# Kernel tuning notes

Hardware: AMD Instinct MI355X
Metric: run time of the kernel (lower is better)

## Reference

```python
import jax, jax.numpy as jnp
import numpy as np

B, T = 16, 512
LAT, ACT, TSK = 512, 64, 96
E, NH, HD = 1024, 16, 64
L, HID, MAXS = 4, 4096, 512


def setup_inputs() -> dict:
    key = jax.random.key(0)
    ks = jax.random.split(key, 16)
    def rn(k, shape, std=0.02):
        return jax.random.normal(k, shape, jnp.float32) * std
    return {
        "z": jax.random.normal(ks[0], (B, T, LAT), jnp.float32),
        "a": jax.random.normal(ks[1], (B, T, ACT), jnp.float32),
        "task_emb": jax.random.normal(ks[2], (B, T, TSK), jnp.float32),
        "input_proj_w": rn(ks[3], (LAT + ACT + TSK, E)),
        "input_proj_b": jnp.zeros((E,), jnp.float32),
        "pos_emb": rn(ks[4], (1, MAXS, E)),
        "ln1_w": jnp.ones((L, E), jnp.float32),
        "ln1_b": jnp.zeros((L, E), jnp.float32),
        "qkv_w": rn(ks[5], (L, E, 3 * E)),
        "proj_w": rn(ks[6], (L, E, E)),
        "proj_b": jnp.zeros((L, E), jnp.float32),
        "ln2_w": jnp.ones((L, E), jnp.float32),
        "ln2_b": jnp.zeros((L, E), jnp.float32),
        "mlp_w1": rn(ks[7], (L, E, HID)),
        "mlp_b1": jnp.zeros((L, HID), jnp.float32),
        "mlp_w2": rn(ks[8], (L, HID, E)),
        "mlp_b2": jnp.zeros((L, E), jnp.float32),
        "out_norm_w": jnp.ones((E,), jnp.float32),
        "out_norm_b": jnp.zeros((E,), jnp.float32),
        "delta_w": rn(ks[9], (E, LAT)),
        "delta_b": jnp.zeros((LAT,), jnp.float32),
    }


def _ln(x, w, b, eps=1e-5):
    mu = jnp.mean(x, -1, keepdims=True)
    var = jnp.mean((x - mu) ** 2, -1, keepdims=True)
    return (x - mu) * jax.lax.rsqrt(var + eps) * w + b


def reference(z, a, task_emb, input_proj_w, input_proj_b, pos_emb,
              ln1_w, ln1_b, qkv_w, proj_w, proj_b, ln2_w, ln2_b,
              mlp_w1, mlp_b1, mlp_w2, mlp_b2,
              out_norm_w, out_norm_b, delta_w, delta_b):
    Bv, Tv, _ = z.shape
    x = jnp.concatenate([z, a, task_emb], axis=-1) @ input_proj_w + input_proj_b
    x = x + pos_emb[:, :Tv]
    scale = HD ** -0.5
    causal = jnp.tril(jnp.ones((Tv, Tv), bool))  # seq_start=0, no cache
    for l in range(L):
        h = _ln(x, ln1_w[l], ln1_b[l])
        qkv = (h @ qkv_w[l]).reshape(Bv, Tv, 3, NH, HD)
        q = jnp.swapaxes(qkv[:, :, 0], 1, 2) * scale  # (B,H,T,D)
        k = jnp.swapaxes(qkv[:, :, 1], 1, 2)
        v = jnp.swapaxes(qkv[:, :, 2], 1, 2)
        attn = jnp.einsum('bhqd,bhkd->bhqk', q, k)
        attn = jnp.where(causal, attn, -jnp.inf)
        attn = jax.nn.softmax(attn, axis=-1)
        o = jnp.einsum('bhqk,bhkd->bhqd', attn, v)
        o = jnp.swapaxes(o, 1, 2).reshape(Bv, Tv, E)
        x = x + (o @ proj_w[l] + proj_b[l])
        h2 = _ln(x, ln2_w[l], ln2_b[l])
        mid = jax.nn.gelu(h2 @ mlp_w1[l] + mlp_b1[l], approximate=False)
        x = x + (mid @ mlp_w2[l] + mlp_b2[l])
    x = _ln(x, out_norm_w, out_norm_b)
    return z + (x @ delta_w + delta_b)
```

## Files before the change

kernel.cpp:

```cpp
#include <hip/hip_runtime.h>
#include <hip/hip_bf16.h>
#include <math.h>

typedef unsigned short u16;
typedef unsigned int u32;
typedef __attribute__((ext_vector_type(4))) float f32x4;
typedef __attribute__((ext_vector_type(8))) short bf16x8;

#define DEV static __device__ __forceinline__

DEV u16 f2bf(float f) {
  __hip_bfloat16 h = __float2bfloat16(f);
  union { __hip_bfloat16 h; u16 u; } c; c.h = h; return c.u;
}

DEV float fast_gelu(float v) {
  float u = v * (1.5957691216f + 0.0713548162f * v * v);
  return v * __builtin_amdgcn_rcpf(1.f + __expf(-u));
}

DEV void gload16(const void* g, void* l) {
  __builtin_amdgcn_global_load_lds((const __attribute__((address_space(1))) u32*)g,
                                   (__attribute__((address_space(3))) u32*)l, 16, 0, 0);
}

__global__ void transpose_w(const float* __restrict__ src, u16* __restrict__ dst,
                            int R, int C, int Rp, size_t sstride, size_t dstride) {
  src += (size_t)blockIdx.z * sstride;
  dst += (size_t)blockIdx.z * dstride;
  __shared__ float tile[32][33];
  int tx = threadIdx.x, ty = threadIdx.y;
  int c0 = blockIdx.x * 32, r0 = blockIdx.y * 32;
  #pragma unroll
  for (int j = 0; j < 4; j++) {
    int r = r0 + ty + j * 8, c = c0 + tx;
    tile[ty + j * 8][tx] = (r < R && c < C) ? src[(size_t)r * C + c] : 0.f;
  }
  __syncthreads();
  #pragma unroll
  for (int j = 0; j < 4; j++) {
    int cc = c0 + ty + j * 8;
    int rr = r0 + tx;
    if (cc < C && rr < Rp) dst[(size_t)cc * Rp + rr] = f2bf(tile[tx][ty + j * 8]);
  }
}

__global__ void concat_k(const float* __restrict__ z, const float* __restrict__ a,
                         const float* __restrict__ te, u16* __restrict__ A) {
  const int total = 8192 * 704;
  for (int idx = blockIdx.x * 256 + threadIdx.x; idx < total; idx += gridDim.x * 256) {
    int m = idx / 704;
    int j = idx - m * 704;
    float v = 0.f;
    if (j < 512) v = z[(size_t)m * 512 + j];
    else if (j < 576) v = a[(size_t)m * 64 + (j - 512)];
    else if (j < 672) v = te[(size_t)m * 96 + (j - 576)];
    A[idx] = f2bf(v);
  }
}

__global__ __launch_bounds__(256) void ln_k(const float* __restrict__ x,
                                            const float* __restrict__ w,
                                            const float* __restrict__ b,
                                            u16* __restrict__ h) {
  int row = blockIdx.x * 4 + (threadIdx.x >> 6);
  int lane = threadIdx.x & 63;
  const float4* xr = (const float4*)(x + (size_t)row * 1024);
  float4 v[4]; float s = 0.f, sq = 0.f;
  #pragma unroll
  for (int i = 0; i < 4; i++) {
    v[i] = xr[lane + i * 64];
    s += v[i].x + v[i].y + v[i].z + v[i].w;
    sq += v[i].x * v[i].x + v[i].y * v[i].y + v[i].z * v[i].z + v[i].w * v[i].w;
  }
  #pragma unroll
  for (int off = 32; off >= 1; off >>= 1) { s += __shfl_xor(s, off); sq += __shfl_xor(sq, off); }
  float mean = s * (1.f / 1024.f);
  float var = sq * (1.f / 1024.f) - mean * mean;
  float rstd = rsqrtf(var + 1e-5f);
  const float4* wv = (const float4*)w;
  const float4* bv = (const float4*)b;
  u32* hr = (u32*)(h + (size_t)row * 1024);
  #pragma unroll
  for (int i = 0; i < 4; i++) {
    int idx = lane + i * 64;
    float4 wi = wv[idx], bi = bv[idx];
    float o0 = (v[i].x - mean) * rstd * wi.x + bi.x;
    float o1 = (v[i].y - mean) * rstd * wi.y + bi.y;
    float o2 = (v[i].z - mean) * rstd * wi.z + bi.z;
    float o3 = (v[i].w - mean) * rstd * wi.w + bi.w;
    hr[idx * 2]     = (u32)f2bf(o0) | ((u32)f2bf(o1) << 16);
    hr[idx * 2 + 1] = (u32)f2bf(o2) | ((u32)f2bf(o3) << 16);
  }
}

template <int FM, int EPI>
__global__ __launch_bounds__(512, 2) void gemm8(
    const u16* __restrict__ A, const u16* __restrict__ BT,
    float* __restrict__ outF, u16* __restrict__ outH,
    const float* __restrict__ bias, const float* __restrict__ res,
    const float* __restrict__ pos, int M, int N, int K, int gx) {
  constexpr int BM = FM * 32;
  constexpr int ABYTES = BM * 64;
  constexpr int BBYTES = 256 * 64;
  constexpr int SLICE = ABYTES + BBYTES;
  constexpr int LA = ABYTES / 8192;
  constexpr int LB = 2;
  __shared__ char lds[4 * SLICE];

  const int tid = threadIdx.x, lane = tid & 63, w = tid >> 6;
  const int wr = w >> 2, wc = w & 3;

  const int nwg = gridDim.x, orig = blockIdx.x;
  const int q = nwg >> 3, r = nwg & 7;
  const int xcd = orig & 7, loc = orig >> 3;
  const int sid = (xcd < r ? xcd * (q + 1) : r * (q + 1) + (xcd - r) * q) + loc;
  const int m0 = (sid / gx) * BM, n0 = (sid % gx) * 256;

  const char* Ag = (const char*)(A + (size_t)m0 * K);
  const char* Bg = (const char*)(BT + (size_t)n0 * K);
  const int Krow = K * 2;

  int aoff[LA], boff[LB];
  #pragma unroll
  for (int l = 0; l < LA; l++) {
    int c = l * 512 + tid, rw = c >> 2, g = (c & 3) ^ ((rw >> 1) & 3);
    aoff[l] = rw * Krow + g * 16;
  }
  #pragma unroll
  for (int l = 0; l < LB; l++) {
    int c = l * 512 + tid, rw = c >> 2, g = (c & 3) ^ ((rw >> 1) & 3);
    boff[l] = rw * Krow + g * 16;
  }
  const int ra = wr * (FM * 16) + (lane & 15);
  const int aRd = ra * 64 + (((lane >> 4) ^ ((ra >> 1) & 3)) << 4);
  const int rb = wc * 64 + (lane & 15);
  const int bRd = rb * 64 + (((lane >> 4) ^ ((rb >> 1) & 3)) << 4);

  f32x4 zero4 = {0.f, 0.f, 0.f, 0.f};
  f32x4 acc[FM][4];
  #pragma unroll
  for (int m = 0; m < FM; m++)
    #pragma unroll
    for (int n = 0; n < 4; n++) acc[m][n] = zero4;

  auto stageA = [&](int s) {
    char* Ad = lds + (s & 3) * SLICE;
    const char* src = Ag + (size_t)s * 64;
    #pragma unroll
    for (int l = 0; l < LA; l++)
      gload16(src + aoff[l], Ad + (l * 512 + w * 64) * 16);
  };
  auto stageB = [&](int s) {
    char* Bd = lds + (s & 3) * SLICE + ABYTES;
    const char* src = Bg + (size_t)s * 64;
    #pragma unroll
    for (int l = 0; l < LB; l++)
      gload16(src + boff[l], Bd + (l * 512 + w * 64) * 16);
  };

  const int NS = K >> 5;
  stageA(0); stageB(0); stageA(1); stageB(1);
  asm volatile("s_waitcnt vmcnt(3)" ::: "memory");
  __builtin_amdgcn_s_barrier();

  #pragma unroll 1
  for (int s = 0; s < NS; s++) {
    char* Ar = lds + (s & 3) * SLICE;
    char* Br = Ar + ABYTES;
    const bool pre = (s + 2 < NS);
    bf16x8 bfr[4], af[4];
    #pragma unroll
    for (int n = 0; n < 4; n++) bfr[n] = *(const bf16x8*)(Br + bRd + n * 1024);
    #pragma unroll
    for (int m = 0; m < 4; m++) af[m] = *(const bf16x8*)(Ar + aRd + m * 1024);
    if (pre) { stageA(s + 2); stageB(s + 2); }
    __builtin_amdgcn_sched_barrier(0);
    __builtin_amdgcn_s_barrier();
    asm volatile("s_waitcnt lgkmcnt(0)" ::: "memory");
    __builtin_amdgcn_sched_barrier(0);
    __builtin_amdgcn_s_setprio(1);
    #pragma unroll
    for (int m = 0; m < 4; m++)
      #pragma unroll
      for (int n = 0; n < 4; n++)
        acc[m][n] = __builtin_amdgcn_mfma_f32_16x16x32_bf16(af[m], bfr[n], acc[m][n], 0, 0, 0);
    __builtin_amdgcn_s_setprio(0);
    __builtin_amdgcn_sched_barrier(0);
    if (pre) asm volatile("s_waitcnt vmcnt(3)" ::: "memory");
    else     asm volatile("s_waitcnt vmcnt(0)" ::: "memory");
    __builtin_amdgcn_s_barrier();
  }

  #pragma unroll
  for (int m = 0; m < FM; m++) {
    #pragma unroll
    for (int i = 0; i < 4; i++) {
      int gm = m0 + wr * (FM * 16) + m * 16 + ((lane >> 4) << 2) + i;
      #pragma unroll
      for (int n = 0; n < 4; n++) {
        int gn = n0 + wc * 64 + n * 16 + (lane & 15);
        float v = acc[m][n][i];
        if (EPI & 1) v += bias[gn];
        if (EPI & 2) v += pos[(size_t)(gm & 511) * N + gn];
        if (EPI & 4) v += res[(size_t)gm * N + gn];
        if (EPI & 8) v = fast_gelu(v);
        if (EPI & 16) outH[(size_t)gm * N + gn] = f2bf(v);
        else outF[(size_t)gm * N + gn] = v;
      }
    }
  }
}

#define SB0 __builtin_amdgcn_sched_barrier(0)
#define VMW(N) asm volatile("s_waitcnt vmcnt(" #N ")" ::: "memory")
#define PH_TAIL(MFMAS) \
  SB0; __builtin_amdgcn_s_barrier(); \
  asm volatile("s_waitcnt lgkmcnt(0)" ::: "memory"); SB0; \
  __builtin_amdgcn_s_setprio(1); MFMAS; __builtin_amdgcn_s_setprio(0); \
  SB0; __builtin_amdgcn_s_barrier();
#define PH_TAILV(MFMAS, NN) \
  SB0; __builtin_amdgcn_s_barrier(); \
  asm volatile("s_waitcnt lgkmcnt(0)" ::: "memory"); SB0; \
  __builtin_amdgcn_s_setprio(1); MFMAS; __builtin_amdgcn_s_setprio(0); \
  SB0; VMW(NN); __builtin_amdgcn_s_barrier();
#define MM16(MB, BF) \
  _Pragma("unroll") \
  for (int mm = 0; mm < 4; mm++) \
    _Pragma("unroll") \
    for (int nn = 0; nn < 4; nn++) \
      acc[(MB) + mm][nn] = __builtin_amdgcn_mfma_f32_16x16x32_bf16(afr[mm][0], BF[nn], acc[(MB) + mm][nn], 0, 0, 0);
#define MM32(MB) \
  _Pragma("unroll") \
  for (int kk2 = 0; kk2 < 2; kk2++) \
    _Pragma("unroll") \
    for (int mm = 0; mm < 4; mm++) \
      _Pragma("unroll") \
      for (int nn = 0; nn < 4; nn++) \
        acc[(MB) + mm][nn] = __builtin_amdgcn_mfma_f32_16x16x32_bf16( \
            afr[mm][kk2], kk2 ? bfr1[nn] : bfr0[nn], acc[(MB) + mm][nn], 0, 0, 0);
#define RD_A1(BUF, K2L, MB) { \
  const char* _b = aRdB[BUF]; \
  afr[0][0] = *(const bf16x8*)(_b + aby[(MB) + 0][K2L]); \
  afr[1][0] = *(const bf16x8*)(_b + aby[(MB) + 1][K2L]); \
  afr[2][0] = *(const bf16x8*)(_b + aby[(MB) + 2][K2L]); \
  afr[3][0] = *(const bf16x8*)(_b + aby[(MB) + 3][K2L]); }
#define RD_A8(BUF, MB) { \
  const char* _b = aRdB[BUF]; \
  afr[0][0] = *(const bf16x8*)(_b + aby[(MB) + 0][0]); \
  afr[0][1] = *(const bf16x8*)(_b + aby[(MB) + 0][1]); \
  afr[1][0] = *(const bf16x8*)(_b + aby[(MB) + 1][0]); \
  afr[1][1] = *(const bf16x8*)(_b + aby[(MB) + 1][1]); \
  afr[2][0] = *(const bf16x8*)(_b + aby[(MB) + 2][0]); \
  afr[2][1] = *(const bf16x8*)(_b + aby[(MB) + 2][1]); \
  afr[3][0] = *(const bf16x8*)(_b + aby[(MB) + 3][0]); \
  afr[3][1] = *(const bf16x8*)(_b + aby[(MB) + 3][1]); }
#define RD_BALL(BUF) { \
  const char* _b = bRdB[BUF]; \
  bfr0[0] = *(const bf16x8*)(_b + bby[0][0]); bfr1[0] = *(const bf16x8*)(_b + bby[0][1]); \
  bfr0[1] = *(const bf16x8*)(_b + bby[1][0]); bfr1[1] = *(const bf16x8*)(_b + bby[1][1]); \
  bfr0[2] = *(const bf16x8*)(_b + bby[2][0]); bfr1[2] = *(const bf16x8*)(_b + bby[2][1]); \
  bfr0[3] = *(const bf16x8*)(_b + bby[3][0]); bfr1[3] = *(const bf16x8*)(_b + bby[3][1]); }

template <int FM, int EPI>
__global__ __launch_bounds__(512, 2) void gemmP(
    const u16* __restrict__ A, const u16* __restrict__ BT,
    float* __restrict__ outF, u16* __restrict__ outH,
    const float* __restrict__ bias, const float* __restrict__ res,
    const float* __restrict__ pos, int M, int N, int K, int gx) {
  constexpr int RB = 16384;
  constexpr int NAREG = (FM == 8 ? 4 : 2);
  constexpr int BOFF = NAREG * RB;
  __shared__ char lds[BOFF + 4 * RB];

  const int tid = threadIdx.x, lane = tid & 63, w = tid >> 6;
  const int wr = w >> 2, wc = w & 3;
  const int ln = lane & 15, g = lane >> 4;

  const int nwg = gridDim.x, orig = blockIdx.x;
  const int q = nwg >> 3, r = nwg & 7;
  const int xcd = orig & 7, loc = orig >> 3;
  const int sid = (xcd < r ? xcd * (q + 1) : r * (q + 1) + (xcd - r) * q) + loc;
  const int m0 = (sid / gx) * (FM * 32), n0 = (sid % gx) * 256;

  const char* Ag = (const char*)(A + (size_t)m0 * K);
  const char* Bg = (const char*)(BT + (size_t)n0 * K);
  const size_t K2 = (size_t)K * 2;
  const int NT = K >> 6, NTm1 = NT - 1, NI = NT >> 1;

  int aby[FM][2], bby[4][2];
  #pragma unroll
  for (int m = 0; m < FM; m++) {
    int rr = (FM == 8 ? 0 : wr * 64) + m * 16 + ln;
    #pragma unroll
    for (int k2 = 0; k2 < 2; k2++)
      aby[m][k2] = rr * 128 + (((k2 * 4 + g) ^ (rr & 7)) << 4);
  }
  #pragma unroll
  for (int n = 0; n < 4; n++) {
    int rr = (wc & 1) * 64 + n * 16 + ln;
    #pragma unroll
    for (int k2 = 0; k2 < 2; k2++)
      bby[n][k2] = rr * 128 + (((k2 * 4 + g) ^ (rr & 7)) << 4);
  }
  const char* aRdB[2];
  const char* bRdB[2];
  if constexpr (FM == 8) {
    aRdB[0] = lds + (0 * 2 + wr) * RB;
    aRdB[1] = lds + (1 * 2 + wr) * RB;
  } else {
    aRdB[0] = lds;
    aRdB[1] = lds + RB;
  }
  bRdB[0] = lds + BOFF + (0 * 2 + (wc >> 1)) * RB;
  bRdB[1] = lds + BOFF + (1 * 2 + (wc >> 1)) * RB;

  int soff[2], sdst[2];
  #pragma unroll
  for (int l = 0; l < 2; l++) {
    int c = l * 512 + tid, rw = c >> 3, sl = c & 7;
    soff[l] = rw * (int)K2 + ((sl ^ (rw & 7)) << 4);
    sdst[l] = (l * 512 + w * 64) * 16;
  }

  auto stA = [&](int buf, int tau, int h) {
    char* d = lds + (FM == 8 ? (buf * 2 + h) : buf) * RB;
    const char* s = Ag + (size_t)(tau < NT ? tau : NTm1) * 128 + (FM == 8 ? (size_t)h * 128 * K2 : 0);
    #pragma unroll
    for (int l = 0; l < 2; l++) gload16(s + soff[l], d + sdst[l]);
  };
  auto stB = [&](int buf, int tau, int gg) {
    char* d = lds + BOFF + (buf * 2 + gg) * RB;
    const char* s = Bg + (size_t)(tau < NT ? tau : NTm1) * 128 + (size_t)gg * 128 * K2;
    #pragma unroll
    for (int l = 0; l < 2; l++) gload16(s + soff[l], d + sdst[l]);
  };

  f32x4 zero4 = {0.f, 0.f, 0.f, 0.f};
  f32x4 acc[FM][4];
  #pragma unroll
  for (int m = 0; m < FM; m++)
    #pragma unroll
    for (int n = 0; n < 4; n++) acc[m][n] = zero4;

  bf16x8 afr[4][2], bfr0[4], bfr1[4];

  if constexpr (FM == 8) {
    stA(0, 0, 0); stA(0, 0, 1); stB(0, 0, 0); stB(0, 0, 1); stB(1, 1, 0); stB(1, 1, 1);
    VMW(4);
    __builtin_amdgcn_s_barrier();
    #pragma unroll 1
    for (int J = 0; J < NI; J++) {
      const int t = 2 * J;
      RD_BALL(0); RD_A8(0, 0); stA(1, t + 1, 0); stA(1, t + 1, 1);
      PH_TAIL(MM32(0));
      RD_A8(0, 4); stB(0, t + 2, 0); stB(0, t + 2, 1);
      PH_TAILV(MM32(4), 4);
      RD_BALL(1); RD_A8(1, 0); stA(0, t + 2, 0); stA(0, t + 2, 1);
      PH_TAIL(MM32(0));
      RD_A8(1, 4); stB(1, t + 3, 0); stB(1, t + 3, 1);
      PH_TAILV(MM32(4), 4);
    }
  } else {
    stA(0, 0, 0); stB(0, 0, 0); stB(0, 0, 1); stB(1, 1, 0); stB(1, 1, 1);
    VMW(4);
    __builtin_amdgcn_s_barrier();
    #pragma unroll 1
    for (int J = 0; J < NI; J++) {
      const int t = 2 * J;
      RD_BALL(0); RD_A1(0, 0, 0); stA(1, t + 1, 0);
      PH_TAIL(MM16(0, bfr0));
      RD_A1(0, 1, 0); stB(0, t + 2, 0);
      PH_TAILV(MM16(0, bfr1), 2);
      RD_BALL(1); RD_A1(1, 0, 0); stB(0, t + 2, 1); stA(0, t + 2, 0);
      PH_TAIL(MM16(0, bfr0));
      RD_A1(1, 1, 0); stB(1, t + 3, 0); stB(1, t + 3, 1);
      PH_TAILV(MM16(0, bfr1), 4);
    }
  }
  VMW(0);

  #pragma unroll
  for (int m = 0; m < FM; m++) {
    #pragma unroll
    for (int i = 0; i < 4; i++) {
      int gm = m0 + wr * (FM * 16) + m * 16 + (g << 2) + i;
      #pragma unroll
      for (int n = 0; n < 4; n++) {
        int gn = n0 + wc * 64 + n * 16 + ln;
        float v = acc[m][n][i];
        if (EPI & 1) v += bias[gn];
        if (EPI & 2) v += pos[(size_t)(gm & 511) * N + gn];
        if (EPI & 4) v += res[(size_t)gm * N + gn];
        if (EPI & 8) v = fast_gelu(v);
        if (EPI & 16) outH[(size_t)gm * N + gn] = f2bf(v);
        else outF[(size_t)gm * N + gn] = v;
      }
    }
  }
}
#undef RD_BALL
#undef RD_A8
#undef RD_A1
#undef MM32
#undef MM16
#undef PH_TAILV
#undef PH_TAIL
#undef VMW
#undef SB0

__global__ __launch_bounds__(512) void attn_k(const u16* __restrict__ qkv,
                                              u16* __restrict__ o) {
  __shared__ u16 Ks[512 * 64];
  __shared__ u16 Vt[64 * 512];
  __shared__ u16 Ps[8 * 1024];
  const int tid = threadIdx.x, lane = tid & 63, w = tid >> 6;
  const int b = blockIdx.x >> 4, h = blockIdx.x & 15;
  const u16* base = qkv + (size_t)b * 512 * 3072 + h * 64;
  const int ln = lane & 15, g = lane >> 4;

  #pragma unroll
  for (int it = 0; it < 8; it++) {
    int chunk = it * 512 + tid;
    int row = chunk >> 3;
    int ib = (chunk & 7) * 16;
    int lb = ib ^ ((row & 7) << 4);
    gload16((const char*)(base + 1024 + (size_t)row * 3072) + lb,
            (char*)Ks + (it * 512 + w * 64) * 16);
  }
  {
    const u16* vrow = base + 2048 + (size_t)tid * 3072;
    #pragma unroll
    for (int c = 0; c < 8; c++) {
      uint4 u = *(const uint4*)(vrow + c * 8);
      u32 vals[4] = {u.x, u.y, u.z, u.w};
      #pragma unroll
      for (int pc = 0; pc < 4; pc++) {
        int d0 = c * 8 + pc * 2;
        size_t by0 = ((size_t)d0 * 1024 + tid * 2) ^ (size_t)((d0 & 7) << 4);
        size_t by1 = ((size_t)(d0 + 1) * 1024 + tid * 2) ^ (size_t)(((d0 + 1) & 7) << 4);
        *(u16*)((char*)Vt + by0) = (u16)(vals[pc] & 0xffff);
        *(u16*)((char*)Vt + by1) = (u16)(vals[pc] >> 16);
      }
    }
  }
  __syncthreads();

  const int qts[4] = {w, 15 - w, 16 + w, 31 - w};
  #pragma unroll
  for (int qi = 0; qi < 4; qi++) {
    const int qt = qts[qi];
    const int q0 = qt * 16;
    const int qcol = q0 + ln;
    const u16* qrow = base + (size_t)(q0 + ln) * 3072 + (g << 3);
    bf16x8 qf0 = *(const bf16x8*)qrow;
    bf16x8 qf1 = *(const bf16x8*)(qrow + 32);
    f32x4 zero4 = {0.f, 0.f, 0.f, 0.f};
    f32x4 oA[4] = {zero4, zero4, zero4, zero4};
    float mrun = -INFINITY, lrun = 0.f;
    const int nch = (qt >> 2) + 1;
    for (int ch = 0; ch < nch; ch++) {
      const int kb = ch * 64;
      f32x4 st[4];
      #pragma unroll
      for (int s = 0; s < 4; s++) {
        st[s] = zero4;
        int krow = kb + s * 16 + ln;
        int byc = krow * 128 + (g << 4);
        int sw = (krow & 7) << 4;
        bf16x8 ka  = *(const bf16x8*)((const char*)Ks + (byc ^ sw));
        bf16x8 kb2 = *(const bf16x8*)((const char*)Ks + ((byc + 64) ^ sw));
        st[s] = __builtin_amdgcn_mfma_f32_16x16x32_bf16(ka, qf0, st[s], 0, 0, 0);
        st[s] = __builtin_amdgcn_mfma_f32_16x16x32_bf16(kb2, qf1, st[s], 0, 0, 0);
      }
      float sv[16]; float cmax = -INFINITY;
      #pragma unroll
      for (int s = 0; s < 4; s++) {
        #pragma unroll
        for (int i = 0; i < 4; i++) {
          int key0 = kb + s * 16 + (g << 2) + i;
          float v = st[s][i] * 0.125f;
          if (key0 > qcol) v = -INFINITY;
          sv[s * 4 + i] = v;
          cmax = fmaxf(cmax, v);
        }
      }
      cmax = fmaxf(cmax, __shfl_xor(cmax, 16));
      cmax = fmaxf(cmax, __shfl_xor(cmax, 32));
      float mnew = fmaxf(mrun, cmax);
      float corr = __expf(mrun - mnew);
      float pp[16]; float psum = 0.f;
      #pragma unroll
      for (int i = 0; i < 16; i++) { pp[i] = __expf(sv[i] - mnew); psum += pp[i]; }
      psum += __shfl_xor(psum, 16);
      psum += __shfl_xor(psum, 32);
      lrun = lrun * corr + psum;
      mrun = mnew;
      {
        int sw2 = (ln & 3) << 4;
        #pragma unroll
        for (int hh = 0; hh < 2; hh++) {
          int pbase = w * 2048 + hh * 1024 + ln * 64;
          uint2 t0, t1;
          t0.x = (u32)f2bf(pp[8 * hh + 0]) | ((u32)f2bf(pp[8 * hh + 1]) << 16);
          t0.y = (u32)f2bf(pp[8 * hh + 2]) | ((u32)f2bf(pp[8 * hh + 3]) << 16);
          t1.x = (u32)f2bf(pp[8 * hh + 4]) | ((u32)f2bf(pp[8 * hh + 5]) << 16);
          t1.y = (u32)f2bf(pp[8 * hh + 6]) | ((u32)f2bf(pp[8 * hh + 7]) << 16);
          *(uint2*)((char*)Ps + pbase + ((g << 3) ^ sw2)) = t0;
          *(uint2*)((char*)Ps + pbase + ((32 + (g << 3)) ^ sw2)) = t1;
        }
      }
      #pragma unroll
      for (int i = 0; i < 4; i++) {
        float fi = __shfl(corr, (g << 2) + i);
        oA[0][i] *= fi; oA[1][i] *= fi; oA[2][i] *= fi; oA[3][i] *= fi;
      }
      {
        int sw2 = (ln & 3) << 4;
        #pragma unroll
        for (int hh = 0; hh < 2; hh++) {
          bf16x8 pf = *(const bf16x8*)((const char*)Ps + w * 2048 + hh * 1024 +
                                       ln * 64 + ((g << 4) ^ sw2));
          #pragma unroll
          for (int n = 0; n < 4; n++) {
            int d = n * 16 + ln;
            int vby = (d * 1024 + (kb + 32 * hh + (g << 3)) * 2) ^ ((d & 7) << 4);
            bf16x8 vf = *(const bf16x8*)((const char*)Vt + vby);
            oA[n] = __builtin_amdgcn_mfma_f32_16x16x32_bf16(pf, vf, oA[n], 0, 0, 0);
          }
        }
      }
    }
    float inv = 1.f / lrun;
    #pragma unroll
    for (int i = 0; i < 4; i++) {
      float fi = __shfl(inv, (g << 2) + i);
      int qr = q0 + (g << 2) + i;
      size_t orow = ((size_t)b * 512 + qr) * 1024 + h * 64;
      #pragma unroll
      for (int n = 0; n < 4; n++)
        o[orow + n * 16 + ln] = f2bf(oA[n][i] * fi);
    }
  }
}

extern "C" void kernel_launch(void* const* d_in, const int* in_sizes, int n_in,
                              void* d_out, int out_size, void* d_ws, size_t ws_size,
                              hipStream_t stream) {
  const float* z    = (const float*)d_in[0];
  const float* a    = (const float*)d_in[1];
  const float* te   = (const float*)d_in[2];
  const float* ipw  = (const float*)d_in[3];
  const float* ipb  = (const float*)d_in[4];
  const float* pos  = (const float*)d_in[5];
  const float* ln1w = (const float*)d_in[6];
  const float* ln1b = (const float*)d_in[7];
  const float* qkvw = (const float*)d_in[8];
  const float* projw= (const float*)d_in[9];
  const float* projb= (const float*)d_in[10];
  const float* ln2w = (const float*)d_in[11];
  const float* ln2b = (const float*)d_in[12];
  const float* w1   = (const float*)d_in[13];
  const float* b1   = (const float*)d_in[14];
  const float* w2   = (const float*)d_in[15];
  const float* b2   = (const float*)d_in[16];
  const float* onw  = (const float*)d_in[17];
  const float* onb  = (const float*)d_in[18];
  const float* dw   = (const float*)d_in[19];
  const float* db   = (const float*)d_in[20];
  float* out = (float*)d_out;

  char* p = (char*)d_ws;
  auto alloc = [&](size_t bytes) -> char* {
    char* r = p; p += (bytes + 255) & ~(size_t)255; return r;
  };
  u16* wt_in   = (u16*)alloc((size_t)1024 * 704 * 2);
  u16* wt_qkv  = (u16*)alloc((size_t)4 * 3072 * 1024 * 2);
  u16* wt_proj = (u16*)alloc((size_t)4 * 1024 * 1024 * 2);
  u16* wt_m1   = (u16*)alloc((size_t)4 * 4096 * 1024 * 2);
  u16* wt_m2   = (u16*)alloc((size_t)4 * 1024 * 4096 * 2);
  u16* wt_d    = (u16*)alloc((size_t)512 * 1024 * 2);
  u16* abuf    = (u16*)alloc((size_t)8192 * 704 * 2);
  float* xbuf  = (float*)alloc((size_t)8192 * 1024 * 4);
  u16* hbuf    = (u16*)alloc((size_t)8192 * 1024 * 2);
  u16* big     = (u16*)alloc((size_t)8192 * 4096 * 2);
  u16* obuf    = (u16*)alloc((size_t)8192 * 1024 * 2);
  u16* qkvb = big;
  u16* mid  = big;

  dim3 tb(32, 8);
  transpose_w<<<dim3(32, 22, 1), tb, 0, stream>>>(ipw, wt_in, 672, 1024, 704, 0, 0);
  transpose_w<<<dim3(96, 32, 4), tb, 0, stream>>>(qkvw, wt_qkv, 1024, 3072, 1024,
      (size_t)1024 * 3072, (size_t)3072 * 1024);
  transpose_w<<<dim3(32, 32, 4), tb, 0, stream>>>(projw, wt_proj, 1024, 1024, 1024,
      (size_t)1024 * 1024, (size_t)1024 * 1024);
  transpose_w<<<dim3(128, 32, 4), tb, 0, stream>>>(w1, wt_m1, 1024, 4096, 1024,
      (size_t)1024 * 4096, (size_t)4096 * 1024);
  transpose_w<<<dim3(32, 128, 4), tb, 0, stream>>>(w2, wt_m2, 4096, 1024, 4096,
      (size_t)4096 * 1024, (size_t)1024 * 4096);
  transpose_w<<<dim3(16, 32, 1), tb, 0, stream>>>(dw, wt_d, 1024, 512, 1024, 0, 0);

  concat_k<<<4096, 256, 0, stream>>>(z, a, te, abuf);

  gemm8<4, 3><<<4 * 64, 512, 0, stream>>>(abuf, wt_in, xbuf, nullptr, ipb, nullptr, pos, 8192, 1024, 704, 4);

  for (int l = 0; l < 4; l++) {
    ln_k<<<2048, 256, 0, stream>>>(xbuf, ln1w + l * 1024, ln1b + l * 1024, hbuf);
    gemmP<8, 16><<<384, 512, 0, stream>>>(hbuf, wt_qkv + (size_t)l * 3072 * 1024, nullptr, qkvb, nullptr, nullptr, nullptr, 8192, 3072, 1024, 12);
    attn_k<<<256, 512, 0, stream>>>(qkvb, obuf);
    gemmP<4, 5><<<256, 512, 0, stream>>>(obuf, wt_proj + (size_t)l * 1024 * 1024, xbuf, nullptr, projb + l * 1024, xbuf, nullptr, 8192, 1024, 1024, 4);
    ln_k<<<2048, 256, 0, stream>>>(xbuf, ln2w + l * 1024, ln2b + l * 1024, hbuf);
    gemmP<8, 25><<<512, 512, 0, stream>>>(hbuf, wt_m1 + (size_t)l * 4096 * 1024, nullptr, mid, b1 + l * 4096, nullptr, nullptr, 8192, 4096, 1024, 16);
    gemmP<4, 5><<<256, 512, 0, stream>>>(mid, wt_m2 + (size_t)l * 1024 * 4096, xbuf, nullptr, b2 + l * 1024, xbuf, nullptr, 8192, 1024, 4096, 4);
  }
  ln_k<<<2048, 256, 0, stream>>>(xbuf, onw, onb, hbuf);
  gemmP<4, 5><<<128, 512, 0, stream>>>(hbuf, wt_d, out, nullptr, db, z, nullptr, 8192, 512, 1024, 2);
}
```

Measured before the change: 1.334 ms.

## Replace phased GEMM with 3-stage K32 ring-buffer kernel using fixed 128x256 tiles

Swaps the two-phase gemmP (256-row or 128-row tiles, K=64 per stage, double buffering) for gemmD. The new kernel always uses 128x256 tiles, K=32 per stage and a three-slice LDS ring with one barrier per step, and declares 4 blocks per CU in its launch bounds. QKV and MLP1 now launch twice as many blocks with smaller M tiles. The aim is more occupancy and simpler sync to hide latency. In exchange, A and B reuse per tile drops, and the shorter K step means more barriers relative to MFMA work.

After: 1.381 ms. 3.5% more time.

```diff
diff --git a/kernel.cpp b/kernel.cpp
--- a/kernel.cpp
+++ b/kernel.cpp
@@ -212,66 +212,14 @@
   }
 }
 
-#define SB0 __builtin_amdgcn_sched_barrier(0)
-#define VMW(N) asm volatile("s_waitcnt vmcnt(" #N ")" ::: "memory")
-#define PH_TAIL(MFMAS) \
-  SB0; __builtin_amdgcn_s_barrier(); \
-  asm volatile("s_waitcnt lgkmcnt(0)" ::: "memory"); SB0; \
-  __builtin_amdgcn_s_setprio(1); MFMAS; __builtin_amdgcn_s_setprio(0); \
-  SB0; __builtin_amdgcn_s_barrier();
-#define PH_TAILV(MFMAS, NN) \
-  SB0; __builtin_amdgcn_s_barrier(); \
-  asm volatile("s_waitcnt lgkmcnt(0)" ::: "memory"); SB0; \
-  __builtin_amdgcn_s_setprio(1); MFMAS; __builtin_amdgcn_s_setprio(0); \
-  SB0; VMW(NN); __builtin_amdgcn_s_barrier();
-#define MM16(MB, BF) \
-  _Pragma("unroll") \
-  for (int mm = 0; mm < 4; mm++) \
-    _Pragma("unroll") \
-    for (int nn = 0; nn < 4; nn++) \
-      acc[(MB) + mm][nn] = __builtin_amdgcn_mfma_f32_16x16x32_bf16(afr[mm][0], BF[nn], acc[(MB) + mm][nn], 0, 0, 0);
-#define MM32(MB) \
-  _Pragma("unroll") \
-  for (int kk2 = 0; kk2 < 2; kk2++) \
-    _Pragma("unroll") \
-    for (int mm = 0; mm < 4; mm++) \
-      _Pragma("unroll") \
-      for (int nn = 0; nn < 4; nn++) \
-        acc[(MB) + mm][nn] = __builtin_amdgcn_mfma_f32_16x16x32_bf16( \
-            afr[mm][kk2], kk2 ? bfr1[nn] : bfr0[nn], acc[(MB) + mm][nn], 0, 0, 0);
-#define RD_A1(BUF, K2L, MB) { \
-  const char* _b = aRdB[BUF]; \
-  afr[0][0] = *(const bf16x8*)(_b + aby[(MB) + 0][K2L]); \
-  afr[1][0] = *(const bf16x8*)(_b + aby[(MB) + 1][K2L]); \
-  afr[2][0] = *(const bf16x8*)(_b + aby[(MB) + 2][K2L]); \
-  afr[3][0] = *(const bf16x8*)(_b + aby[(MB) + 3][K2L]); }
-#define RD_A8(BUF, MB) { \
-  const char* _b = aRdB[BUF]; \
-  afr[0][0] = *(const bf16x8*)(_b + aby[(MB) + 0][0]); \
-  afr[0][1] = *(const bf16x8*)(_b + aby[(MB) + 0][1]); \
-  afr[1][0] = *(const bf16x8*)(_b + aby[(MB) + 1][0]); \
-  afr[1][1] = *(const bf16x8*)(_b + aby[(MB) + 1][1]); \
-  afr[2][0] = *(const bf16x8*)(_b + aby[(MB) + 2][0]); \
-  afr[2][1] = *(const bf16x8*)(_b + aby[(MB) + 2][1]); \
-  afr[3][0] = *(const bf16x8*)(_b + aby[(MB) + 3][0]); \
-  afr[3][1] = *(const bf16x8*)(_b + aby[(MB) + 3][1]); }
-#define RD_BALL(BUF) { \
-  const char* _b = bRdB[BUF]; \
-  bfr0[0] = *(const bf16x8*)(_b + bby[0][0]); bfr1[0] = *(const bf16x8*)(_b + bby[0][1]); \
-  bfr0[1] = *(const bf16x8*)(_b + bby[1][0]); bfr1[1] = *(const bf16x8*)(_b + bby[1][1]); \
-  bfr0[2] = *(const bf16x8*)(_b + bby[2][0]); bfr1[2] = *(const bf16x8*)(_b + bby[2][1]); \
-  bfr0[3] = *(const bf16x8*)(_b + bby[3][0]); bfr1[3] = *(const bf16x8*)(_b + bby[3][1]); }
-
-template <int FM, int EPI>
-__global__ __launch_bounds__(512, 2) void gemmP(
+template <int EPI>
+__global__ __launch_bounds__(512, 4) void gemmD(
     const u16* __restrict__ A, const u16* __restrict__ BT,
     float* __restrict__ outF, u16* __restrict__ outH,
     const float* __restrict__ bias, const float* __restrict__ res,
     const float* __restrict__ pos, int M, int N, int K, int gx) {
-  constexpr int RB = 16384;
-  constexpr int NAREG = (FM == 8 ? 4 : 2);
-  constexpr int BOFF = NAREG * RB;
-  __shared__ char lds[BOFF + 4 * RB];
+  constexpr int SLICE = 24576;
+  __shared__ char lds[3 * SLICE];
 
   const int tid = threadIdx.x, lane = tid & 63, w = tid >> 6;
   const int wr = w >> 2, wc = w & 3;
@@ -281,110 +229,80 @@
   const int q = nwg >> 3, r = nwg & 7;
   const int xcd = orig & 7, loc = orig >> 3;
   const int sid = (xcd < r ? xcd * (q + 1) : r * (q + 1) + (xcd - r) * q) + loc;
-  const int m0 = (sid / gx) * (FM * 32), n0 = (sid % gx) * 256;
+  const int m0 = (sid / gx) * 128, n0 = (sid % gx) * 256;
 
   const char* Ag = (const char*)(A + (size_t)m0 * K);
   const char* Bg = (const char*)(BT + (size_t)n0 * K);
-  const size_t K2 = (size_t)K * 2;
-  const int NT = K >> 6, NTm1 = NT - 1, NI = NT >> 1;
-
-  int aby[FM][2], bby[4][2];
-  #pragma unroll
-  for (int m = 0; m < FM; m++) {
-    int rr = (FM == 8 ? 0 : wr * 64) + m * 16 + ln;
-    #pragma unroll
-    for (int k2 = 0; k2 < 2; k2++)
-      aby[m][k2] = rr * 128 + (((k2 * 4 + g) ^ (rr & 7)) << 4);
-  }
-  #pragma unroll
-  for (int n = 0; n < 4; n++) {
-    int rr = (wc & 1) * 64 + n * 16 + ln;
-    #pragma unroll
-    for (int k2 = 0; k2 < 2; k2++)
-      bby[n][k2] = rr * 128 + (((k2 * 4 + g) ^ (rr & 7)) << 4);
-  }
-  const char* aRdB[2];
-  const char* bRdB[2];
-  if constexpr (FM == 8) {
-    aRdB[0] = lds + (0 * 2 + wr) * RB;
-    aRdB[1] = lds + (1 * 2 + wr) * RB;
-  } else {
-    aRdB[0] = lds;
-    aRdB[1] = lds + RB;
-  }
-  bRdB[0] = lds + BOFF + (0 * 2 + (wc >> 1)) * RB;
-  bRdB[1] = lds + BOFF + (1 * 2 + (wc >> 1)) * RB;
-
-  int soff[2], sdst[2];
-  #pragma unroll
-  for (int l = 0; l < 2; l++) {
-    int c = l * 512 + tid, rw = c >> 3, sl = c & 7;
-    soff[l] = rw * (int)K2 + ((sl ^ (rw & 7)) << 4);
-    sdst[l] = (l * 512 + w * 64) * 16;
-  }
-
-  auto stA = [&](int buf, int tau, int h) {
-    char* d = lds + (FM == 8 ? (buf * 2 + h) : buf) * RB;
-    const char* s = Ag + (size_t)(tau < NT ? tau : NTm1) * 128 + (FM == 8 ? (size_t)h * 128 * K2 : 0);
-    #pragma unroll
-    for (int l = 0; l < 2; l++) gload16(s + soff[l], d + sdst[l]);
+  const int K2 = K * 2;
+  const int NS = K >> 5, NSm1 = NS - 1;
+
+  const int slotR = (g ^ (ln & 3)) << 4;
+  int aby[4], bby[4];
+  #pragma unroll
+  for (int m = 0; m < 4; m++) aby[m] = (wr * 64 + m * 16 + ln) * 64 + slotR;
+  #pragma unroll
+  for (int n = 0; n < 4; n++)
+    bby[n] = 8192 + (wc >> 1) * 8192 + ((wc & 1) * 64 + n * 16 + ln) * 64 + slotR;
+
+  const int arw = tid >> 2, asl = tid & 3;
+  const int aoff = arw * K2 + ((asl ^ (arw & 3)) << 4);
+  const int brw1 = 128 + (tid >> 2);
+  const int boff0 = aoff;
+  const int boff1 = brw1 * K2 + ((asl ^ (brw1 & 3)) << 4);
+
+  auto stage = [&](int sl3, int tau) {
+    int tt = tau < NS ? tau : NSm1;
+    char* base = lds + sl3 * SLICE;
+    const char* sa = Ag + (size_t)tt * 64;
+    const char* sb = Bg + (size_t)tt * 64;
+    gload16(sa + aoff, base + tid * 16);
+    gload16(sb + boff0, base + 8192 + tid * 16);
+    gload16(sb + boff1, base + 8192 + (512 + tid) * 16);
   };
-  auto stB = [&](int buf, int tau, int gg) {
-    char* d = lds + BOFF + (buf * 2 + gg) * RB;
-    const char* s = Bg + (size_t)(tau < NT ? tau : NTm1) * 128 + (size_t)gg * 128 * K2;
-    #pragma unroll
-    for (int l = 0; l < 2; l++) gload16(s + soff[l], d + sdst[l]);
-  };
 
   f32x4 zero4 = {0.f, 0.f, 0.f, 0.f};
-  f32x4 acc[FM][4];
-  #pragma unroll
-  for (int m = 0; m < FM; m++)
+  f32x4 acc[4][4];
+  #pragma unroll
+  for (int m = 0; m < 4; m++)
     #pragma unroll
     for (int n = 0; n < 4; n++) acc[m][n] = zero4;
 
-  bf16x8 afr[4][2], bfr0[4], bfr1[4];
-
-  if constexpr (FM == 8) {
-    stA(0, 0, 0); stA(0, 0, 1); stB(0, 0, 0); stB(0, 0, 1); stB(1, 1, 0); stB(1, 1, 1);
-    VMW(4);
+  bf16x8 afr[4], bfr[4];
+
+  stage(0, 0); stage(1, 1);
+  asm volatile("s_waitcnt vmcnt(3)" ::: "memory");
+  __builtin_amdgcn_s_barrier();
+
+  int s0 = 0, s1 = 1, s2 = 2;
+  #pragma unroll 1
+  for (int s = 0; s < NS; s++) {
+    const char* base = lds + s0 * SLICE;
+    stage(s2, s + 2);
+    #pragma unroll
+    for (int n = 0; n < 4; n++) bfr[n] = *(const bf16x8*)(base + bby[n]);
+    #pragma unroll
+    for (int m = 0; m < 4; m++) afr[m] = *(const bf16x8*)(base + aby[m]);
+    __builtin_amdgcn_sched_barrier(0);
+    asm volatile("s_waitcnt lgkmcnt(0)" ::: "memory");
+    __builtin_amdgcn_sched_barrier(0);
+    __builtin_amdgcn_s_setprio(1);
+    #pragma unroll
+    for (int m = 0; m < 4; m++)
+      #pragma unroll
+      for (int n = 0; n < 4; n++)
+        acc[m][n] = __builtin_amdgcn_mfma_f32_16x16x32_bf16(afr[m], bfr[n], acc[m][n], 0, 0, 0);
+    __builtin_amdgcn_s_setprio(0);
+    __builtin_amdgcn_sched_barrier(0);
+    asm volatile("s_waitcnt vmcnt(3)" ::: "memory");
     __builtin_amdgcn_s_barrier();
-    #pragma unroll 1
-    for (int J = 0; J < NI; J++) {
-      const int t = 2 * J;
-      RD_BALL(0); RD_A8(0, 0); stA(1, t + 1, 0); stA(1, t + 1, 1);
-      PH_TAIL(MM32(0));
-      RD_A8(0, 4); stB(0, t + 2, 0); stB(0, t + 2, 1);
-      PH_TAILV(MM32(4), 4);
-      RD_BALL(1); RD_A8(1, 0); stA(0, t + 2, 0); stA(0, t + 2, 1);
-      PH_TAIL(MM32(0));
-      RD_A8(1, 4); stB(1, t + 3, 0); stB(1, t + 3, 1);
-      PH_TAILV(MM32(4), 4);
-    }
-  } else {
-    stA(0, 0, 0); stB(0, 0, 0); stB(0, 0, 1); stB(1, 1, 0); stB(1, 1, 1);
-    VMW(4);
-    __builtin_amdgcn_s_barrier();
-    #pragma unroll 1
-    for (int J = 0; J < NI; J++) {
-      const int t = 2 * J;
-      RD_BALL(0); RD_A1(0, 0, 0); stA(1, t + 1, 0);
-      PH_TAIL(MM16(0, bfr0));
-      RD_A1(0, 1, 0); stB(0, t + 2, 0);
-      PH_TAILV(MM16(0, bfr1), 2);
-      RD_BALL(1); RD_A1(1, 0, 0); stB(0, t + 2, 1); stA(0, t + 2, 0);
-      PH_TAIL(MM16(0, bfr0));
-      RD_A1(1, 1, 0); stB(1, t + 3, 0); stB(1, t + 3, 1);
-      PH_TAILV(MM16(0, bfr1), 4);
-    }
-  }
-  VMW(0);
-
-  #pragma unroll
-  for (int m = 0; m < FM; m++) {
+    int t = s0; s0 = s1; s1 = s2; s2 = t;
+  }
+
+  #pragma unroll
+  for (int m = 0; m < 4; m++) {
     #pragma unroll
     for (int i = 0; i < 4; i++) {
-      int gm = m0 + wr * (FM * 16) + m * 16 + (g << 2) + i;
+      int gm = m0 + wr * 64 + m * 16 + (g << 2) + i;
       #pragma unroll
       for (int n = 0; n < 4; n++) {
         int gn = n0 + wc * 64 + n * 16 + ln;
@@ -399,15 +317,6 @@
     }
   }
 }
-#undef RD_BALL
-#undef RD_A8
-#undef RD_A1
-#undef MM32
-#undef MM16
-#undef PH_TAILV
-#undef PH_TAIL
-#undef VMW
-#undef SB0
 
 __global__ __launch_bounds__(512) void attn_k(const u16* __restrict__ qkv,
                                               u16* __restrict__ o) {
@@ -606,13 +515,13 @@
 
   for (int l = 0; l < 4; l++) {
     ln_k<<<2048, 256, 0, stream>>>(xbuf, ln1w + l * 1024, ln1b + l * 1024, hbuf);
-    gemmP<8, 16><<<384, 512, 0, stream>>>(hbuf, wt_qkv + (size_t)l * 3072 * 1024, nullptr, qkvb, nullptr, nullptr, nullptr, 8192, 3072, 1024, 12);
+    gemmD<16><<<768, 512, 0, stream>>>(hbuf, wt_qkv + (size_t)l * 3072 * 1024, nullptr, qkvb, nullptr, nullptr, nullptr, 8192, 3072, 1024, 12);
     attn_k<<<256, 512, 0, stream>>>(qkvb, obuf);
-    gemmP<4, 5><<<256, 512, 0, stream>>>(obuf, wt_proj + (size_t)l * 1024 * 1024, xbuf, nullptr, projb + l * 1024, xbuf, nullptr, 8192, 1024, 1024, 4);
+    gemmD<5><<<256, 512, 0, stream>>>(obuf, wt_proj + (size_t)l * 1024 * 1024, xbuf, nullptr, projb + l * 1024, xbuf, nullptr, 8192, 1024, 1024, 4);
     ln_k<<<2048, 256, 0, stream>>>(xbuf, ln2w + l * 1024, ln2b + l * 1024, hbuf);
-    gemmP<8, 25><<<512, 512, 0, stream>>>(hbuf, wt_m1 + (size_t)l * 4096 * 1024, nullptr, mid, b1 + l * 4096, nullptr, nullptr, 8192, 4096, 1024, 16);
-    gemmP<4, 5><<<256, 512, 0, stream>>>(mid, wt_m2 + (size_t)l * 1024 * 4096, xbuf, nullptr, b2 + l * 1024, xbuf, nullptr, 8192, 1024, 4096, 4);
+    gemmD<25><<<1024, 512, 0, stream>>>(hbuf, wt_m1 + (size_t)l * 4096 * 1024, nullptr, mid, b1 + l * 4096, nullptr, nullptr, 8192, 4096, 1024, 16);
+    gemmD<5><<<256, 512, 0, stream>>>(mid, wt_m2 + (size_t)l * 1024 * 4096, xbuf, nullptr, b2 + l * 1024, xbuf, nullptr, 8192, 1024, 4096, 4);
   }
   ln_k<<<2048, 256, 0, stream>>>(xbuf, onw, onb, hbuf);
-  gemmP<4, 5><<<128, 512, 0, stream>>>(hbuf, wt_d, out, nullptr, db, z, nullptr, 8192, 512, 1024, 2);
-}
+  gemmD<5><<<128, 512, 0, stream>>>(hbuf, wt_d, out, nullptr, db, z, nullptr, 8192, 512, 1024, 2);
+}
```
